# Kernel optimization log

Measured on AMD Instinct MI355X. Metric: run time of the kernel, lower is better.

## Reference

```python
import jax, jax.numpy as jnp
import numpy as np

S, NL = 64, 5000          # num_sequences, num_labels
PD, LD = 1024, 768        # protein / label embedding dims
DIM, OD = 512, 512        # latent_dim, output_dim


def setup_inputs() -> dict:
    key = jax.random.key(0)
    ks = jax.random.split(key, 8)
    sc = lambda f: 1.0 / np.sqrt(f).astype(np.float32)
    return {
        "P_f": jax.random.normal(ks[0], (S, PD), jnp.float32),
        "label_emb": jax.random.normal(ks[1], (NL, LD), jnp.float32),
        "W_p": jax.random.normal(ks[2], (DIM, PD), jnp.float32) * sc(PD),
        "W_l": jax.random.normal(ks[3], (DIM, LD), jnp.float32) * sc(LD),
        "W1": jax.random.normal(ks[4], (OD, 2 * DIM), jnp.float32) * sc(2 * DIM),
        "b1": jnp.zeros((OD,), jnp.float32),
        "W2": jax.random.normal(ks[5], (OD, OD), jnp.float32) * sc(OD),
        "b2": jnp.zeros((OD,), jnp.float32),
        "W3": jax.random.normal(ks[6], (1, OD), jnp.float32) * sc(OD),
        "b3": jnp.zeros((1,), jnp.float32),
        "L": jnp.arange(NL, dtype=jnp.int64),
    }


def reference(P_f, label_emb, W_p, W_l, W1, b1, W2, b2, W3, b3, L):
    # label lookup (cached_label_embeddings(L)) + linear projections
    L_f = label_emb[L]                      # [NL, LD]
    P_e = P_f @ W_p.T                       # [S, DIM]
    L_e = L_f @ W_l.T                       # [NL, DIM]
    # joint cat([P_e_expanded, L_e_expanded]) @ W1.T  ==  P-side + L-side GEMMs,
    # broadcast-summed (avoids materializing the [S*NL, 2*DIM] concat)
    hp = P_e @ W1[:, :DIM].T                # [S, OD]
    hl = L_e @ W1[:, DIM:].T                # [NL, OD]
    h = jax.nn.relu(hp[:, None, :] + hl[None, :, :] + b1)   # [S, NL, OD]
    h = jax.nn.relu(jnp.einsum("snd,od->sno", h, W2) + b2)  # [S, NL, OD]
    logits = jnp.einsum("sno,o->sn", h, W3[0]) + b3[0]      # [S, NL]
    return logits
```

## Files before the change

### kernel.cpp

```cpp
#include <hip/hip_runtime.h>
#include <hip/hip_bf16.h>

typedef short short8 __attribute__((ext_vector_type(8)));
typedef float f32x4 __attribute__((ext_vector_type(4)));

#define S_   64
#define NL_  5000
#define PD_  1024
#define LD_  768
#define DIM_ 512
#define OD_  512

#define BK     32
#define KT2    8
#define KSTEPS 16
#define NT_M   79
#define HL_RT  157

__device__ __forceinline__ ushort f2bf(float f) {
    union { float f; unsigned u; } v; v.f = f;
    unsigned r = v.u + 0x7fffu + ((v.u >> 16) & 1u);
    return (ushort)(r >> 16);
}
__device__ __forceinline__ float bf2f(ushort h) {
    union { unsigned u; float f; } v; v.u = ((unsigned)h) << 16;
    return v.f;
}
__device__ __forceinline__ int swz(int row, int kslot) {
    return (row * 64 + kslot * 16) ^ (((row >> 1) & 7) << 4);
}

__device__ __forceinline__ void proj8(
    float* Af , const float* __restrict__ A, int lda, int K,
    const float* __restrict__ W, int ldw, const float* __restrict__ bias,
    float* __restrict__ C, int o0, int t) {
    const int s = t & 63, og = t >> 6;
    const int oA = o0 + og * 2, oB = oA + 1;
    float acc0 = 0.f, acc1 = 0.f;
    for (int ck = 0; ck < K; ck += 256) {
        __syncthreads();
#pragma unroll
        for (int it = 0; it < 16; it++) {
            int r = it * 4 + (t >> 6);
            float4 v = *(const float4*)(A + (size_t)r * lda + ck + (t & 63) * 4);
            *(float4*)(Af + r * 258 + (t & 63) * 4) = v;
        }
        __syncthreads();
        const float* w0 = W + (size_t)oA * ldw + ck;
        const float* w1 = W + (size_t)oB * ldw + ck;
        const float* ar = Af + s * 258;
#pragma unroll 8
        for (int k4 = 0; k4 < 64; k4++) {
            f32x4 a4 = *(const f32x4*)(ar + k4 * 4);
            float4 v0 = *(const float4*)(w0 + k4 * 4);
            float4 v1 = *(const float4*)(w1 + k4 * 4);
            acc0 += a4[0] * v0.x + a4[1] * v0.y + a4[2] * v0.z + a4[3] * v0.w;
            acc1 += a4[0] * v1.x + a4[1] * v1.y + a4[2] * v1.z + a4[3] * v1.w;
        }
    }
    C[s * DIM_ + oA] = acc0 + (bias ? bias[oA] : 0.f);
    C[s * DIM_ + oB] = acc1 + (bias ? bias[oB] : 0.f);
}

__global__ __launch_bounds__(256) void k_pre1(
    const float* __restrict__ W2, const float* __restrict__ W_l,
    const float* __restrict__ W1, const float* __restrict__ P_f,
    const float* __restrict__ W_p,
    char* __restrict__ panel, ushort* __restrict__ MlT, float* __restrict__ P_e) {
    __shared__ float lbuf[64 * 258];
    int b = blockIdx.x, t = threadIdx.x;
    if (b < 128) {
        int c = b * 256 + t;
        int o = c >> 6, rem = c & 63, kt = rem >> 2, kslot = rem & 3;
        const float* src = W2 + o * DIM_ + kt * BK + kslot * 8;
        float4 v0 = *(const float4*)src;
        float4 v1 = *(const float4*)(src + 4);
        union { ushort u[8]; short8 v; } pk;
        pk.u[0] = f2bf(v0.x); pk.u[1] = f2bf(v0.y); pk.u[2] = f2bf(v0.z); pk.u[3] = f2bf(v0.w);
        pk.u[4] = f2bf(v1.x); pk.u[5] = f2bf(v1.y); pk.u[6] = f2bf(v1.z); pk.u[7] = f2bf(v1.w);
        *(short8*)(panel + kt * 32768 + (o >> 4) * 1024 + kslot * 256 + (o & 15) * 16) = pk.v;
    } else if (b < 320) {
        float (*w1r)[DIM_] = (float (*)[DIM_])lbuf;
        int bx = b - 128;
        int o0 = (bx / 3) * 8;
        int ld = (bx % 3) * 256 + t;
        for (int i = t; i < 8 * DIM_; i += 256)
            w1r[i >> 9][i & 511] = W1[(o0 + (i >> 9)) * (2 * DIM_) + DIM_ + (i & 511)];
        __syncthreads();
        float acc[8] = {};
        for (int dim = 0; dim < DIM_; dim++) {
            float wl = W_l[dim * LD_ + ld];
#pragma unroll
            for (int oi = 0; oi < 8; oi++) acc[oi] += w1r[oi][dim] * wl;
        }
#pragma unroll
        for (int oi = 0; oi < 8; oi++) MlT[(o0 + oi) * LD_ + ld] = f2bf(acc[oi]);
    } else {
        proj8(lbuf, P_f, PD_, PD_, W_p, PD_, nullptr, P_e, (b - 320) * 8, t);
    }
}

__global__ __launch_bounds__(256) void k_pre2(
    const float* __restrict__ P_e, const float* __restrict__ W1,
    const float* __restrict__ b1, const float* __restrict__ emb,
    const int* __restrict__ L, const ushort* __restrict__ MlT,
    float* __restrict__ hpb, ushort* __restrict__ hlB) {
    __shared__ float lbuf[64 * 258];
    int b = blockIdx.x, t = threadIdx.x;
    if (b < 64) {
        proj8(lbuf, P_e, DIM_, DIM_, W1, 2 * DIM_, b1, hpb, b * 8, t);
    } else {
        int hb = b - 64;
        int rblk = hb % HL_RT, oh = hb / HL_RT;
        int r0 = rblk * 32;
        int w = t >> 6, l = t & 63, lg = l >> 4, ll = l & 15;
        const float* arow[2];
#pragma unroll
        for (int mt = 0; mt < 2; mt++) {
            int r = r0 + mt * 16 + ll;
            if (r >= NL_) r = NL_ - 1;
            arow[mt] = emb + (size_t)L[r] * LD_ + lg * 8;
        }
        f32x4 acc[2][4] = {};
        for (int k = 0; k < LD_; k += 32) {
            short8 a[2], bf[4];
#pragma unroll
            for (int mt = 0; mt < 2; mt++) {
                float4 v0 = *(const float4*)(arow[mt] + k);
                float4 v1 = *(const float4*)(arow[mt] + k + 4);
                union { ushort u[8]; short8 v; } pk;
                pk.u[0] = f2bf(v0.x); pk.u[1] = f2bf(v0.y);
                pk.u[2] = f2bf(v0.z); pk.u[3] = f2bf(v0.w);
                pk.u[4] = f2bf(v1.x); pk.u[5] = f2bf(v1.y);
                pk.u[6] = f2bf(v1.z); pk.u[7] = f2bf(v1.w);
                a[mt] = pk.v;
            }
#pragma unroll
            for (int ot = 0; ot < 4; ot++) {
                int o = oh * 256 + w * 64 + ot * 16 + ll;
                bf[ot] = *(const short8*)(MlT + o * LD_ + k + lg * 8);
            }
#pragma unroll
            for (int mt = 0; mt < 2; mt++)
#pragma unroll
                for (int ot = 0; ot < 4; ot++)
                    acc[mt][ot] = __builtin_amdgcn_mfma_f32_16x16x32_bf16(a[mt], bf[ot], acc[mt][ot], 0, 0, 0);
        }
#pragma unroll
        for (int mt = 0; mt < 2; mt++)
#pragma unroll
            for (int ot = 0; ot < 4; ot++)
#pragma unroll
                for (int reg = 0; reg < 4; reg++) {
                    int r = r0 + mt * 16 + lg * 4 + reg;
                    if (r < NL_)
                        hlB[(size_t)r * DIM_ + oh * 256 + w * 64 + ot * 16 + ll] = f2bf(acc[mt][ot][reg]);
                }
    }
}

__global__ __launch_bounds__(512, 2) void k_main2(
    const ushort* __restrict__ hlB, const float* __restrict__ hpb,
    const char* __restrict__ panel, const float* __restrict__ b2,
    const float* __restrict__ W3, const float* __restrict__ b3,
    float* __restrict__ out) {
    __shared__ f32x4 ldsv[2048];
    char* lds = (char*)ldsv;
    const int t = threadIdx.x;
    const int n0 = blockIdx.x * 64, s0 = blockIdx.y * 2;
    const int w = t >> 6, lane = t & 63, lg = lane >> 4, ll = lane & 15;
    const int wr = w >> 2, wc = w & 3;

    const int arow = t >> 2, akslot = t & 3;
    int an = n0 + (arow & 63); if (an >= NL_) an = NL_ - 1;
    const ushort* hlsrc = hlB + (size_t)an * DIM_ + akslot * 8;
    const float*  hpsrc = hpb + (s0 + (arow >> 6)) * DIM_ + akslot * 8;
    const int awz = swz(arow, akslot);

    const int abase = swz(wr * 64 + ll, lg);
    const char* bbase = panel + (wc * 8) * 1024 + lane * 16;

    f32x4 acc[4][8] = {};

    auto packSub = [&](int buf, int sub, short8 hv, f32x4 p0, f32x4 p1) {
        float x[8];
#pragma unroll
        for (int e = 0; e < 4; e++) {
            float a0 = bf2f((ushort)hv[e]) + p0[e];
            float a1 = bf2f((ushort)hv[4 + e]) + p1[e];
            x[e]     = a0 > 0.f ? a0 : 0.f;
            x[4 + e] = a1 > 0.f ? a1 : 0.f;
        }
        union { __hip_bfloat162 h2[4]; short8 v; } pk;
#pragma unroll
        for (int e = 0; e < 4; e++)
            pk.h2[e] = __float22bfloat162_rn(make_float2(x[2 * e], x[2 * e + 1]));
        *(short8*)(lds + buf * 16384 + sub * 8192 + awz) = pk.v;
    };

    {
        short8 hv0 = *(const short8*)(hlsrc);
        short8 hv1 = *(const short8*)(hlsrc + BK);
        f32x4 p00 = *(const f32x4*)(hpsrc);
        f32x4 p01 = *(const f32x4*)(hpsrc + 4);
        f32x4 p10 = *(const f32x4*)(hpsrc + BK);
        f32x4 p11 = *(const f32x4*)(hpsrc + BK + 4);
        packSub(0, 0, hv0, p00, p01);
        packSub(0, 1, hv1, p10, p11);
        asm volatile("s_waitcnt lgkmcnt(0)" ::: "memory");
        __builtin_amdgcn_s_barrier();
    }
    short8 bq0[4], bq1[4];
#pragma unroll
    for (int j = 0; j < 4; j++) bq0[j] = *(const short8*)(bbase + j * 1024);

    for (int kt2 = 0; kt2 < KT2; kt2++) {
        const char* bs0 = bbase + (2 * kt2) * 32768;
        const char* bs1 = bbase + (2 * kt2 + 1) * 32768;
        const char* A = lds + (kt2 & 1) * 16384;
        short8 hv0, hv1; f32x4 p00, p01, p10, p11;
        if (kt2 + 1 < KT2) {
            hv0 = *(const short8*)(hlsrc + (2 * kt2 + 2) * BK);
            hv1 = *(const short8*)(hlsrc + (2 * kt2 + 3) * BK);
            p00 = *(const f32x4*)(hpsrc + (2 * kt2 + 2) * BK);
            p01 = *(const f32x4*)(hpsrc + (2 * kt2 + 2) * BK + 4);
            p10 = *(const f32x4*)(hpsrc + (2 * kt2 + 3) * BK);
            p11 = *(const f32x4*)(hpsrc + (2 * kt2 + 3) * BK + 4);
        }
        short8 a[4];
#pragma unroll
        for (int mt = 0; mt < 4; mt++) a[mt] = *(const short8*)(A + abase + mt * 1024);
#pragma unroll
        for (int j = 0; j < 4; j++) bq1[j] = *(const short8*)(bs0 + 4096 + j * 1024);
        __builtin_amdgcn_s_setprio(1);
#pragma unroll
        for (int mt = 0; mt < 4; mt++)
#pragma unroll
            for (int j = 0; j < 4; j++)
                acc[mt][j] = __builtin_amdgcn_mfma_f32_16x16x32_bf16(a[mt], bq0[j], acc[mt][j], 0, 0, 0);
        __builtin_amdgcn_s_setprio(0);
#pragma unroll
        for (int j = 0; j < 4; j++) bq0[j] = *(const short8*)(bs1 + j * 1024);
        __builtin_amdgcn_s_setprio(1);
#pragma unroll
        for (int mt = 0; mt < 4; mt++)
#pragma unroll
            for (int j = 0; j < 4; j++)
                acc[mt][4 + j] = __builtin_amdgcn_mfma_f32_16x16x32_bf16(a[mt], bq1[j], acc[mt][4 + j], 0, 0, 0);
        __builtin_amdgcn_s_setprio(0);
#pragma unroll
        for (int mt = 0; mt < 4; mt++) a[mt] = *(const short8*)(A + 8192 + abase + mt * 1024);
#pragma unroll
        for (int j = 0; j < 4; j++) bq1[j] = *(const short8*)(bs1 + 4096 + j * 1024);
        __builtin_amdgcn_s_setprio(1);
#pragma unroll
        for (int mt = 0; mt < 4; mt++)
#pragma unroll
            for (int j = 0; j < 4; j++)
                acc[mt][j] = __builtin_amdgcn_mfma_f32_16x16x32_bf16(a[mt], bq0[j], acc[mt][j], 0, 0, 0);
        __builtin_amdgcn_s_setprio(0);
        if (kt2 + 1 < KT2)
#pragma unroll
            for (int j = 0; j < 4; j++)
                bq0[j] = *(const short8*)(bbase + (2 * kt2 + 2) * 32768 + j * 1024);
        __builtin_amdgcn_s_setprio(1);
#pragma unroll
        for (int mt = 0; mt < 4; mt++)
#pragma unroll
            for (int j = 0; j < 4; j++)
                acc[mt][4 + j] = __builtin_amdgcn_mfma_f32_16x16x32_bf16(a[mt], bq1[j], acc[mt][4 + j], 0, 0, 0);
        __builtin_amdgcn_s_setprio(0);
        if (kt2 + 1 < KT2) {
            packSub((kt2 + 1) & 1, 0, hv0, p00, p01);
            packSub((kt2 + 1) & 1, 1, hv1, p10, p11);
        }
        asm volatile("s_waitcnt lgkmcnt(0)" ::: "memory");
        __builtin_amdgcn_s_barrier();
    }

    float* logit = (float*)lds;
    if (t < 128) logit[t] = 0.f;
    __syncthreads();
#pragma unroll
    for (int mt = 0; mt < 4; mt++) {
        float p4[4] = { 0.f, 0.f, 0.f, 0.f };
#pragma unroll
        for (int ot = 0; ot < 8; ot++) {
            int o = wc * 128 + ot * 16 + ll;
            float bb = b2[o], w3 = W3[o];
#pragma unroll
            for (int reg = 0; reg < 4; reg++) {
                float v = acc[mt][ot][reg] + bb;
                v = v > 0.f ? v : 0.f;
                p4[reg] += v * w3;
            }
        }
#pragma unroll
        for (int m = 1; m < 16; m <<= 1)
#pragma unroll
            for (int reg = 0; reg < 4; reg++) p4[reg] += __shfl_xor(p4[reg], m, 64);
        if (ll == 0)
#pragma unroll
            for (int reg = 0; reg < 4; reg++)
                atomicAdd(&logit[wr * 64 + mt * 16 + lg * 4 + reg], p4[reg]);
    }
    __syncthreads();
    if (t < 128) {
        int n = n0 + (t & 63);
        int s = s0 + (t >> 6);
        if (n < NL_) out[(size_t)s * NL_ + n] = logit[t] + b3[0];
    }
}

extern "C" void kernel_launch(void* const* d_in, const int* in_sizes, int n_in,
                              void* d_out, int out_size, void* d_ws, size_t ws_size,
                              hipStream_t stream) {
    const float* P_f = (const float*)d_in[0];
    const float* emb = (const float*)d_in[1];
    const float* W_p = (const float*)d_in[2];
    const float* W_l = (const float*)d_in[3];
    const float* W1  = (const float*)d_in[4];
    const float* b1  = (const float*)d_in[5];
    const float* W2  = (const float*)d_in[6];
    const float* b2  = (const float*)d_in[7];
    const float* W3  = (const float*)d_in[8];
    const float* b3  = (const float*)d_in[9];
    const int*   L   = (const int*)d_in[10];
    float* out = (float*)d_out;

    char* ws = (char*)d_ws;
    size_t off = 0;
    auto alloc = [&](size_t bytes) {
        void* p = ws + off;
        off = (off + bytes + 255) & ~(size_t)255;
        return p;
    };
    char*   panel = (char*)alloc((size_t)KSTEPS * 32768);
    ushort* MlT   = (ushort*)alloc((size_t)OD_ * LD_ * 2);
    float*  P_e   = (float*)alloc((size_t)S_ * DIM_ * 4);
    float*  hpb   = (float*)alloc((size_t)S_ * DIM_ * 4);
    ushort* hlB   = (ushort*)alloc((size_t)NL_ * DIM_ * 2);

    k_pre1<<<384, 256, 0, stream>>>(W2, W_l, W1, P_f, W_p, panel, MlT, P_e);
    k_pre2<<<378, 256, 0, stream>>>(P_e, W1, b1, emb, L, MlT, hpb, hlB);
    k_main2<<<dim3(NT_M, 32), 512, 0, stream>>>(hlB, hpb, panel, b2, W3, b3, out);
}
```

Before: 259.3 us.

## Retile main GEMM per sequence with pre-swizzled hl tiles and async LDS staging

The label-side activations are now written by the pre-kernel straight into a tiled, swizzled layout. The main kernel stages each window into a triple-buffered LDS ring with global_load_lds, and applies the hp-add, ReLU and bf16 pack in registers after reading from LDS. Each block now covers 256 labels × 256 output features for one sequence, so the output dimension is split in two halves. Partial logits go to a workspace and a new small kernel sums them and adds the bias. The goal is to drop the register round-trip used to build the A tile and to overlap loads with MFMA work, at the cost of an extra launch, more LDS per block and some duplicated pack work across waves.

```diff
diff --git a/kernel.cpp b/kernel.cpp
--- a/kernel.cpp
+++ b/kernel.cpp
@@ -12,9 +12,9 @@
 #define OD_  512
 
 #define BK     32
-#define KT2    8
 #define KSTEPS 16
-#define NT_M   79
+#define NWIN   8
+#define NT_A   20
 #define HL_RT  157
 
 __device__ __forceinline__ ushort f2bf(float f) {
@@ -28,6 +28,11 @@
 }
 __device__ __forceinline__ int swz(int row, int kslot) {
     return (row * 64 + kslot * 16) ^ (((row >> 1) & 7) << 4);
+}
+__device__ __forceinline__ void glds16(const void* g, void* l) {
+    __builtin_amdgcn_global_load_lds(
+        (const __attribute__((address_space(1))) void*)g,
+        (__attribute__((address_space(3))) void*)l, 16, 0, 0);
 }
 
 __device__ __forceinline__ void proj8(
@@ -104,7 +109,7 @@
     const float* __restrict__ P_e, const float* __restrict__ W1,
     const float* __restrict__ b1, const float* __restrict__ emb,
     const int* __restrict__ L, const ushort* __restrict__ MlT,
-    float* __restrict__ hpb, ushort* __restrict__ hlB) {
+    float* __restrict__ hpb, char* __restrict__ hlT) {
     __shared__ float lbuf[64 * 258];
     int b = blockIdx.x, t = threadIdx.x;
     if (b < 64) {
@@ -153,36 +158,39 @@
 #pragma unroll
                 for (int reg = 0; reg < 4; reg++) {
                     int r = r0 + mt * 16 + lg * 4 + reg;
-                    if (r < NL_)
-                        hlB[(size_t)r * DIM_ + oh * 256 + w * 64 + ot * 16 + ll] = f2bf(acc[mt][ot][reg]);
+                    int k = oh * 256 + w * 64 + ot * 16 + ll;
+                    if (r < NL_) {
+                        int tile = r >> 8, row = r & 255;
+                        size_t byte = (size_t)tile * 262144 + (k >> 6) * 32768
+                                    + ((k >> 5) & 1) * 16384
+                                    + (size_t)(((row * 64 + ((k >> 3) & 3) * 16)
+                                                ^ (((row >> 1) & 7) << 4)) + (k & 7) * 2);
+                        *(ushort*)(hlT + byte) = f2bf(acc[mt][ot][reg]);
+                    }
                 }
     }
 }
 
 __global__ __launch_bounds__(512, 2) void k_main2(
-    const ushort* __restrict__ hlB, const float* __restrict__ hpb,
+    const char* __restrict__ hlT, const float* __restrict__ hpb,
     const char* __restrict__ panel, const float* __restrict__ b2,
-    const float* __restrict__ W3, const float* __restrict__ b3,
-    float* __restrict__ out) {
-    __shared__ f32x4 ldsv[2048];
+    const float* __restrict__ W3, float* __restrict__ part) {
+    __shared__ f32x4 ldsv[6144];
     char* lds = (char*)ldsv;
     const int t = threadIdx.x;
-    const int n0 = blockIdx.x * 64, s0 = blockIdx.y * 2;
+    const int nt = blockIdx.x, oh = blockIdx.y, s = blockIdx.z;
+    const int n0 = nt * 256;
     const int w = t >> 6, lane = t & 63, lg = lane >> 4, ll = lane & 15;
-    const int wr = w >> 2, wc = w & 3;
-
-    const int arow = t >> 2, akslot = t & 3;
-    int an = n0 + (arow & 63); if (an >= NL_) an = NL_ - 1;
-    const ushort* hlsrc = hlB + (size_t)an * DIM_ + akslot * 8;
-    const float*  hpsrc = hpb + (s0 + (arow >> 6)) * DIM_ + akslot * 8;
-    const int awz = swz(arow, akslot);
-
+    const int wr = w >> 1, wc = w & 1;
+
+    const char* asrc = hlT + (size_t)nt * 262144;
+    const float* hpsrc = hpb + s * DIM_ + lg * 8;
+    const char* bbase = panel + (oh * 16 + wc * 8) * 1024 + lane * 16;
     const int abase = swz(wr * 64 + ll, lg);
-    const char* bbase = panel + (wc * 8) * 1024 + lane * 16;
 
     f32x4 acc[4][8] = {};
 
-    auto packSub = [&](int buf, int sub, short8 hv, f32x4 p0, f32x4 p1) {
+    auto packF = [&](short8 hv, f32x4 p0, f32x4 p1) -> short8 {
         float x[8];
 #pragma unroll
         for (int e = 0; e < 4; e++) {
@@ -195,98 +203,100 @@
 #pragma unroll
         for (int e = 0; e < 4; e++)
             pk.h2[e] = __float22bfloat162_rn(make_float2(x[2 * e], x[2 * e + 1]));
-        *(short8*)(lds + buf * 16384 + sub * 8192 + awz) = pk.v;
+        return pk.v;
     };
-
-    {
-        short8 hv0 = *(const short8*)(hlsrc);
-        short8 hv1 = *(const short8*)(hlsrc + BK);
-        f32x4 p00 = *(const f32x4*)(hpsrc);
-        f32x4 p01 = *(const f32x4*)(hpsrc + 4);
-        f32x4 p10 = *(const f32x4*)(hpsrc + BK);
-        f32x4 p11 = *(const f32x4*)(hpsrc + BK + 4);
-        packSub(0, 0, hv0, p00, p01);
-        packSub(0, 1, hv1, p10, p11);
-        asm volatile("s_waitcnt lgkmcnt(0)" ::: "memory");
+    auto stage = [&](int win) {
+        const char* src = asrc + win * 32768;
+        char* dst = lds + (win % 3) * 32768;
+#pragma unroll
+        for (int i = 0; i < 4; i++)
+            glds16(src + (t + i * 512) * 16, dst + (t + i * 512) * 16);
+    };
+
+    stage(0);
+    stage(1);
+    f32x4 h00 = *(const f32x4*)(hpsrc);
+    f32x4 h01 = *(const f32x4*)(hpsrc + 4);
+    f32x4 h10 = *(const f32x4*)(hpsrc + 32);
+    f32x4 h11 = *(const f32x4*)(hpsrc + 36);
+    asm volatile("s_waitcnt vmcnt(4)" ::: "memory");
+    __builtin_amdgcn_s_barrier();
+
+    for (int win = 0; win < NWIN; win++) {
+        const char* A = lds + (win % 3) * 32768;
+        const char* bk0 = bbase + (2 * win) * 32768;
+        const char* bk1 = bbase + (2 * win + 1) * 32768;
+        short8 a[4], pa[4], bq0[4], bq1[4];
+#pragma unroll
+        for (int mt = 0; mt < 4; mt++) a[mt] = *(const short8*)(A + abase + mt * 1024);
+#pragma unroll
+        for (int j = 0; j < 4; j++) bq0[j] = *(const short8*)(bk0 + j * 1024);
+#pragma unroll
+        for (int mt = 0; mt < 4; mt++) pa[mt] = packF(a[mt], h00, h01);
+#pragma unroll
+        for (int j = 0; j < 4; j++) bq1[j] = *(const short8*)(bk0 + 4096 + j * 1024);
+        __builtin_amdgcn_s_setprio(1);
+#pragma unroll
+        for (int mt = 0; mt < 4; mt++)
+#pragma unroll
+            for (int j = 0; j < 4; j++)
+                acc[mt][j] = __builtin_amdgcn_mfma_f32_16x16x32_bf16(pa[mt], bq0[j], acc[mt][j], 0, 0, 0);
+        __builtin_amdgcn_s_setprio(0);
+#pragma unroll
+        for (int mt = 0; mt < 4; mt++) a[mt] = *(const short8*)(A + 16384 + abase + mt * 1024);
+        f32x4 n00, n01, n10, n11;
+        if (win + 1 < NWIN) {
+            n00 = *(const f32x4*)(hpsrc + (2 * win + 2) * 32);
+            n01 = *(const f32x4*)(hpsrc + (2 * win + 2) * 32 + 4);
+            n10 = *(const f32x4*)(hpsrc + (2 * win + 3) * 32);
+            n11 = *(const f32x4*)(hpsrc + (2 * win + 3) * 32 + 4);
+        }
+        __builtin_amdgcn_s_setprio(1);
+#pragma unroll
+        for (int mt = 0; mt < 4; mt++)
+#pragma unroll
+            for (int j = 0; j < 4; j++)
+                acc[mt][4 + j] = __builtin_amdgcn_mfma_f32_16x16x32_bf16(pa[mt], bq1[j], acc[mt][4 + j], 0, 0, 0);
+        __builtin_amdgcn_s_setprio(0);
+#pragma unroll
+        for (int j = 0; j < 4; j++) bq0[j] = *(const short8*)(bk1 + j * 1024);
+#pragma unroll
+        for (int mt = 0; mt < 4; mt++) pa[mt] = packF(a[mt], h10, h11);
+#pragma unroll
+        for (int j = 0; j < 4; j++) bq1[j] = *(const short8*)(bk1 + 4096 + j * 1024);
+        __builtin_amdgcn_s_setprio(1);
+#pragma unroll
+        for (int mt = 0; mt < 4; mt++)
+#pragma unroll
+            for (int j = 0; j < 4; j++)
+                acc[mt][j] = __builtin_amdgcn_mfma_f32_16x16x32_bf16(pa[mt], bq0[j], acc[mt][j], 0, 0, 0);
+        __builtin_amdgcn_s_setprio(0);
+        __builtin_amdgcn_s_setprio(1);
+#pragma unroll
+        for (int mt = 0; mt < 4; mt++)
+#pragma unroll
+            for (int j = 0; j < 4; j++)
+                acc[mt][4 + j] = __builtin_amdgcn_mfma_f32_16x16x32_bf16(pa[mt], bq1[j], acc[mt][4 + j], 0, 0, 0);
+        __builtin_amdgcn_s_setprio(0);
+        if (win + 1 < NWIN) { h00 = n00; h01 = n01; h10 = n10; h11 = n11; }
+        if (win + 2 < NWIN) {
+            stage(win + 2);
+            asm volatile("s_waitcnt vmcnt(4) lgkmcnt(0)" ::: "memory");
+        } else {
+            asm volatile("s_waitcnt vmcnt(0) lgkmcnt(0)" ::: "memory");
+        }
         __builtin_amdgcn_s_barrier();
     }
-    short8 bq0[4], bq1[4];
-#pragma unroll
-    for (int j = 0; j < 4; j++) bq0[j] = *(const short8*)(bbase + j * 1024);
-
-    for (int kt2 = 0; kt2 < KT2; kt2++) {
-        const char* bs0 = bbase + (2 * kt2) * 32768;
-        const char* bs1 = bbase + (2 * kt2 + 1) * 32768;
-        const char* A = lds + (kt2 & 1) * 16384;
-        short8 hv0, hv1; f32x4 p00, p01, p10, p11;
-        if (kt2 + 1 < KT2) {
-            hv0 = *(const short8*)(hlsrc + (2 * kt2 + 2) * BK);
-            hv1 = *(const short8*)(hlsrc + (2 * kt2 + 3) * BK);
-            p00 = *(const f32x4*)(hpsrc + (2 * kt2 + 2) * BK);
-            p01 = *(const f32x4*)(hpsrc + (2 * kt2 + 2) * BK + 4);
-            p10 = *(const f32x4*)(hpsrc + (2 * kt2 + 3) * BK);
-            p11 = *(const f32x4*)(hpsrc + (2 * kt2 + 3) * BK + 4);
-        }
-        short8 a[4];
-#pragma unroll
-        for (int mt = 0; mt < 4; mt++) a[mt] = *(const short8*)(A + abase + mt * 1024);
-#pragma unroll
-        for (int j = 0; j < 4; j++) bq1[j] = *(const short8*)(bs0 + 4096 + j * 1024);
-        __builtin_amdgcn_s_setprio(1);
-#pragma unroll
-        for (int mt = 0; mt < 4; mt++)
-#pragma unroll
-            for (int j = 0; j < 4; j++)
-                acc[mt][j] = __builtin_amdgcn_mfma_f32_16x16x32_bf16(a[mt], bq0[j], acc[mt][j], 0, 0, 0);
-        __builtin_amdgcn_s_setprio(0);
-#pragma unroll
-        for (int j = 0; j < 4; j++) bq0[j] = *(const short8*)(bs1 + j * 1024);
-        __builtin_amdgcn_s_setprio(1);
-#pragma unroll
-        for (int mt = 0; mt < 4; mt++)
-#pragma unroll
-            for (int j = 0; j < 4; j++)
-                acc[mt][4 + j] = __builtin_amdgcn_mfma_f32_16x16x32_bf16(a[mt], bq1[j], acc[mt][4 + j], 0, 0, 0);
-        __builtin_amdgcn_s_setprio(0);
-#pragma unroll
-        for (int mt = 0; mt < 4; mt++) a[mt] = *(const short8*)(A + 8192 + abase + mt * 1024);
-#pragma unroll
-        for (int j = 0; j < 4; j++) bq1[j] = *(const short8*)(bs1 + 4096 + j * 1024);
-        __builtin_amdgcn_s_setprio(1);
-#pragma unroll
-        for (int mt = 0; mt < 4; mt++)
-#pragma unroll
-            for (int j = 0; j < 4; j++)
-                acc[mt][j] = __builtin_amdgcn_mfma_f32_16x16x32_bf16(a[mt], bq0[j], acc[mt][j], 0, 0, 0);
-        __builtin_amdgcn_s_setprio(0);
-        if (kt2 + 1 < KT2)
-#pragma unroll
-            for (int j = 0; j < 4; j++)
-                bq0[j] = *(const short8*)(bbase + (2 * kt2 + 2) * 32768 + j * 1024);
-        __builtin_amdgcn_s_setprio(1);
-#pragma unroll
-        for (int mt = 0; mt < 4; mt++)
-#pragma unroll
-            for (int j = 0; j < 4; j++)
-                acc[mt][4 + j] = __builtin_amdgcn_mfma_f32_16x16x32_bf16(a[mt], bq1[j], acc[mt][4 + j], 0, 0, 0);
-        __builtin_amdgcn_s_setprio(0);
-        if (kt2 + 1 < KT2) {
-            packSub((kt2 + 1) & 1, 0, hv0, p00, p01);
-            packSub((kt2 + 1) & 1, 1, hv1, p10, p11);
-        }
-        asm volatile("s_waitcnt lgkmcnt(0)" ::: "memory");
-        __builtin_amdgcn_s_barrier();
-    }
 
     float* logit = (float*)lds;
-    if (t < 128) logit[t] = 0.f;
+    if (t < 256) logit[t] = 0.f;
     __syncthreads();
 #pragma unroll
     for (int mt = 0; mt < 4; mt++) {
         float p4[4] = { 0.f, 0.f, 0.f, 0.f };
 #pragma unroll
         for (int ot = 0; ot < 8; ot++) {
-            int o = wc * 128 + ot * 16 + ll;
+            int o = oh * 256 + wc * 128 + ot * 16 + ll;
             float bb = b2[o], w3 = W3[o];
 #pragma unroll
             for (int reg = 0; reg < 4; reg++) {
@@ -305,11 +315,17 @@
                 atomicAdd(&logit[wr * 64 + mt * 16 + lg * 4 + reg], p4[reg]);
     }
     __syncthreads();
-    if (t < 128) {
-        int n = n0 + (t & 63);
-        int s = s0 + (t >> 6);
-        if (n < NL_) out[(size_t)s * NL_ + n] = logit[t] + b3[0];
-    }
+    if (t < 256) {
+        int n = n0 + t;
+        if (n < NL_)
+            part[(size_t)oh * (S_ * NL_) + (size_t)s * NL_ + n] = logit[t];
+    }
+}
+
+__global__ void k_comb(const float* __restrict__ part, const float* __restrict__ b3,
+                       float* __restrict__ out) {
+    int i = blockIdx.x * 256 + threadIdx.x;
+    if (i < S_ * NL_) out[i] = part[i] + part[S_ * NL_ + i] + b3[0];
 }
 
 extern "C" void kernel_launch(void* const* d_in, const int* in_sizes, int n_in,
@@ -339,9 +355,11 @@
     ushort* MlT   = (ushort*)alloc((size_t)OD_ * LD_ * 2);
     float*  P_e   = (float*)alloc((size_t)S_ * DIM_ * 4);
     float*  hpb   = (float*)alloc((size_t)S_ * DIM_ * 4);
-    ushort* hlB   = (ushort*)alloc((size_t)NL_ * DIM_ * 2);
+    char*   hlT   = (char*)alloc((size_t)NT_A * 262144);
+    float*  part  = (float*)alloc((size_t)2 * S_ * NL_ * 4);
 
     k_pre1<<<384, 256, 0, stream>>>(W2, W_l, W1, P_f, W_p, panel, MlT, P_e);
-    k_pre2<<<378, 256, 0, stream>>>(P_e, W1, b1, emb, L, MlT, hpb, hlB);
-    k_main2<<<dim3(NT_M, 32), 512, 0, stream>>>(hlB, hpb, panel, b2, W3, b3, out);
-}
+    k_pre2<<<378, 256, 0, stream>>>(P_e, W1, b1, emb, L, MlT, hpb, hlT);
+    k_main2<<<dim3(NT_A, 2, S_), 512, 0, stream>>>(hlT, hpb, panel, b2, W3, part);
+    k_comb<<<(S_ * NL_ + 255) / 256, 256, 0, stream>>>(part, b3, out);
+}
```

After: 293.1 us. +13.0%, slower.
